# Kernel tuning notes

Measured on AMD Instinct MI355X. Metric: run time of the kernel, lower is better.

Reference implementation:

```python
import jax, jax.numpy as jnp
import numpy as np

KNOTS = 17  # integration points on [0, 3]


def _buffers():
    t = jnp.linspace(0.0, 3.0, KNOTS, dtype=jnp.float32)
    dt = 3.0 / (KNOTS - 1)
    w = jnp.full((KNOTS,), 2.0 * dt, dtype=jnp.float32)
    w = w.at[0].set(dt).at[-1].set(dt)          # trapezoid-style end weights
    phi = jnp.exp(-jnp.square(t) / 2.0)         # ideal Gaussian ECF
    return t, phi, w * phi


def setup_inputs() -> dict:
    key = jax.random.key(0)
    k1, k2 = jax.random.split(key)
    N, D, P = 8192, 512, 1024
    z = jax.random.normal(k1, (N, D), dtype=jnp.float32)
    A = jax.random.normal(k2, (D, P), dtype=jnp.float32)  # random projections (hoisted from forward)
    return {"z": z, "A": A}


def reference(z, A):
    t, phi, weights = _buffers()
    D = z.shape[-1]
    flat = z.reshape(-1, D).astype(jnp.float32)            # [N, D]
    An = A / jnp.clip(jnp.linalg.norm(A, axis=0, keepdims=True), 1e-8)
    proj = flat @ An                                       # [N, P]
    x_t = proj[:, :, None] * t                             # [N, P, K]
    cos_mean = jnp.mean(jnp.cos(x_t), axis=0)              # [P, K]
    sin_mean = jnp.mean(jnp.sin(x_t), axis=0)              # [P, K]
    err = jnp.square(cos_mean - phi) + jnp.square(sin_mean)
    statistic = (err @ weights) * flat.shape[0]            # [P]
    return jnp.mean(statistic)
```

## Files before the change

### kernel.cpp

```cpp
#include <hip/hip_runtime.h>
#include <stdint.h>

#define N_SAMP 8192
#define D_DIM  512
#define P_DIM  1024
#define DT     0.1875f

typedef float f32x4 __attribute__((ext_vector_type(4)));
typedef float f32x2 __attribute__((ext_vector_type(2)));
typedef short bf16x8 __attribute__((ext_vector_type(8)));
typedef unsigned short u16;

__device__ __forceinline__ u16 f2bf(float x){
    unsigned int u = __float_as_uint(x);
    return (u16)((u + 0x7FFFu + ((u >> 16) & 1u)) >> 16);
}

__device__ __forceinline__ void load_lds16(const void* g, void* l){
    __builtin_amdgcn_global_load_lds(
        (const __attribute__((address_space(1))) void*)(uintptr_t)g,
        (__attribute__((address_space(3))) void*)(uint32_t)(uintptr_t)l,
        16, 0, 0);
}

__global__ __launch_bounds__(256) void k_zconv(const float4* __restrict__ z4,
                                               u16* __restrict__ zb,
                                               float* __restrict__ out){
    int i = blockIdx.x * 256 + threadIdx.x;
    if (i == 0) out[0] = 0.f;
    float4 v = z4[i];
    ushort4 o;
    o.x = f2bf(v.x); o.y = f2bf(v.y); o.z = f2bf(v.z); o.w = f2bf(v.w);
    ((ushort4*)zb)[i] = o;
}

__global__ __launch_bounds__(256) void k_norm(const float* __restrict__ A,
                                              float* __restrict__ inv){
    const float4* A4 = (const float4*)A;
    const int tid = threadIdx.x;
    const int q = tid & 7;
    const int g = tid >> 3;
    const int c = (blockIdx.x << 3) + q;
    float sx = 0.f, sy = 0.f, sz = 0.f, sw = 0.f;
    #pragma unroll 4
    for (int dd = 0; dd < 16; ++dd){
        float4 v = A4[(size_t)(g * 16 + dd) * 256 + c];
        sx += v.x * v.x; sy += v.y * v.y; sz += v.z * v.z; sw += v.w * v.w;
    }
    __shared__ float red[8][32][4];
    red[q][g][0] = sx; red[q][g][1] = sy; red[q][g][2] = sz; red[q][g][3] = sw;
    __syncthreads();
    if (tid < 32){
        int qq = tid >> 2, comp = tid & 3;
        float s = 0.f;
        #pragma unroll
        for (int gg = 0; gg < 32; ++gg) s += red[qq][gg][comp];
        float nrm = fmaxf(sqrtf(s), 1e-8f);
        inv[(c - q + qq) * 4 + comp] = 1.0f / nrm;
    }
}

__global__ __launch_bounds__(256) void k_trans(const float* __restrict__ A,
                                               const float* __restrict__ inv,
                                               u16* __restrict__ AnT){
    __shared__ float tile[32][33];
    int p0 = (blockIdx.x & 31) * 32;
    int d0 = (blockIdx.x >> 5) * 32;
    int tx = threadIdx.x & 31, ty = threadIdx.x >> 5;
    #pragma unroll
    for (int j = 0; j < 4; ++j){
        int dd = ty + j * 8;
        tile[dd][tx] = A[(size_t)(d0 + dd) * P_DIM + p0 + tx];
    }
    __syncthreads();
    #pragma unroll
    for (int j = 0; j < 4; ++j){
        int pp = ty + j * 8;
        float s = inv[p0 + pp];
        AnT[(size_t)(p0 + pp) * D_DIM + d0 + tx] = f2bf(tile[tx][pp] * s);
    }
}

__global__ __launch_bounds__(256) void k_gemm_ecf(const u16* __restrict__ zb,
                                                  const u16* __restrict__ AnT,
                                                  float* __restrict__ partial){
    __shared__ uint4 smem4[4096];
    const int tid = threadIdx.x;
    const int bm = blockIdx.x >> 3, bn = blockIdx.x & 7;
    const int m0 = bm << 7, n0 = bn << 7;
    const int w = tid >> 6, lane = tid & 63;
    const int r = lane & 15, kg = lane >> 4;
    const int wm = (w >> 1) << 6, wn = (w & 1) << 6;

    const int srow = tid >> 3;
    const int gsw  = ((tid & 7) ^ (srow & 7)) << 3;
    const u16* gA = zb  + (size_t)(m0 + srow) * D_DIM + gsw;
    const u16* gB = AnT + (size_t)(n0 + srow) * D_DIM + gsw;
    char* lbase = (char*)smem4 + w * 1024;

    f32x4 acc[4][4] = {};

    #pragma unroll
    for (int i = 0; i < 4; ++i){
        load_lds16(gA + (size_t)i * 32 * D_DIM, lbase + i * 4096);
        load_lds16(gB + (size_t)i * 32 * D_DIM, lbase + 16384 + i * 4096);
    }

    for (int kt = 0; kt < 8; ++kt){
        const int cur = kt & 1;
        __syncthreads();
        if (kt < 7){
            char* la = lbase + ((kt + 1) & 1) * 32768;
            #pragma unroll
            for (int i = 0; i < 4; ++i){
                load_lds16(gA + (size_t)i * 32 * D_DIM + (kt + 1) * 64, la + i * 4096);
                load_lds16(gB + (size_t)i * 32 * D_DIM + (kt + 1) * 64, la + 16384 + i * 4096);
            }
        }
        const u16* Ab = (const u16*)smem4 + cur * 16384;
        const u16* Bb = Ab + 8192;
        #pragma unroll
        for (int ks = 0; ks < 2; ++ks){
            bf16x8 af[4], bfr[4];
            #pragma unroll
            for (int i = 0; i < 4; ++i)
                af[i] = *(const bf16x8*)&Ab[(wm + i * 16 + r) * 64 +
                                            (((ks * 4 + kg) ^ (r & 7)) << 3)];
            #pragma unroll
            for (int j = 0; j < 4; ++j)
                bfr[j] = *(const bf16x8*)&Bb[(wn + j * 16 + r) * 64 +
                                             (((ks * 4 + kg) ^ (r & 7)) << 3)];
            #pragma unroll
            for (int i = 0; i < 4; ++i)
                #pragma unroll
                for (int j = 0; j < 4; ++j)
                    acc[i][j] = __builtin_amdgcn_mfma_f32_16x16x32_bf16(
                        af[i], bfr[j], acc[i][j], 0, 0, 0);
        }
    }

    __syncthreads();
    float* epil = (float*)smem4;
    #pragma unroll
    for (int jn = 0; jn < 4; ++jn){
        f32x2 sum[16];
        #pragma unroll
        for (int k = 0; k < 16; ++k) sum[k] = (f32x2){0.f, 0.f};
        #pragma unroll
        for (int i = 0; i < 4; ++i){
            #pragma unroll
            for (int q = 0; q < 4; ++q){
                float x = acc[i][jn][q] * DT;
                float c1 = __cosf(x), s1 = __sinf(x);
                float tc = c1 + c1;
                f32x2 prev = {1.f, 0.f};
                f32x2 curv = {c1, s1};
                sum[0] += curv;
                #pragma unroll
                for (int k = 2; k <= 16; ++k){
                    f32x2 nxt = tc * curv - prev;
                    sum[k - 1] += nxt;
                    prev = curv; curv = nxt;
                }
            }
        }
        #pragma unroll
        for (int k = 0; k < 16; ++k){
            f32x2 o;
            o.x = __shfl_xor(sum[k].x, 16); o.y = __shfl_xor(sum[k].y, 16);
            sum[k] += o;
            o.x = __shfl_xor(sum[k].x, 32); o.y = __shfl_xor(sum[k].y, 32);
            sum[k] += o;
        }
        if (lane < 16){
            const int cl = jn * 16 + lane;
            #pragma unroll
            for (int k = 0; k < 16; ++k){
                epil[(w * 32 + k)      * 64 + cl] = sum[k].x;
                epil[(w * 32 + 16 + k) * 64 + cl] = sum[k].y;
            }
        }
    }
    __syncthreads();
    for (int f0 = 0; f0 < 4096; f0 += 256){
        int f = f0 + tid;
        int cl = f & 127, j = f >> 7;
        int whi = cl >> 6, cll = cl & 63;
        float v = epil[(whi * 32 + j) * 64 + cll] +
                  epil[((whi + 2) * 32 + j) * 64 + cll];
        partial[((size_t)bm * 32 + j) * 1024 + n0 + cl] = v;
    }
}

__global__ __launch_bounds__(256) void k_reduce(const float* __restrict__ partial,
                                                float* __restrict__ out){
    const int tid = threadIdx.x;
    const int idx = blockIdx.x * 256 + tid;
    const int p = idx & 1023, j = idx >> 10;
    float s = 0.f;
    #pragma unroll 4
    for (int slot = 0; slot < 64; ++slot)
        s += partial[((size_t)slot * 32 + j) * 1024 + p];
    const int k = (j & 15) + 1;
    float tk = (float)k * DT;
    float phik = expf(-0.5f * tk * tk);
    float wk = ((k == 16) ? DT : 2.f * DT) * phik;
    float mean = s * (1.f / (float)N_SAMP);
    float diff = (j < 16) ? (mean - phik) : mean;
    float term = diff * diff * wk;
    #pragma unroll
    for (int o = 32; o > 0; o >>= 1) term += __shfl_xor(term, o);
    __shared__ float red[4];
    if ((tid & 63) == 0) red[tid >> 6] = term;
    __syncthreads();
    if (tid == 0)
        atomicAdd(out, (red[0] + red[1] + red[2] + red[3]) *
                       ((float)N_SAMP / (float)P_DIM));
}

extern "C" void kernel_launch(void* const* d_in, const int* in_sizes, int n_in,
                              void* d_out, int out_size, void* d_ws, size_t ws_size,
                              hipStream_t stream){
    const float* z = (const float*)d_in[0];
    const float* A = (const float*)d_in[1];
    char* ws = (char*)d_ws;
    float* inv     = (float*)(ws);
    u16*   AnT     = (u16*)  (ws + 8192);
    u16*   zb      = (u16*)  (ws + 1056768);
    float* partial = (float*)(ws + 9445376);
    float* out     = (float*)d_out;

    hipLaunchKernelGGL(k_zconv,    dim3(4096), dim3(256), 0, stream,
                       (const float4*)z, zb, out);
    hipLaunchKernelGGL(k_norm,     dim3(32),   dim3(256), 0, stream, A, inv);
    hipLaunchKernelGGL(k_trans,    dim3(512),  dim3(256), 0, stream, A, inv, AnT);
    hipLaunchKernelGGL(k_gemm_ecf, dim3(512),  dim3(256), 0, stream, zb, AnT, partial);
    hipLaunchKernelGGL(k_reduce,   dim3(128),  dim3(256), 0, stream, partial, out);
}
```

Measured before the change: 49.76 us.

## Fuse prep kernels, load B fragments directly from global, split reduce across lanes

Merges the z conversion, column-norm and transpose kernels into one launch, with 32 extra blocks each computing norms for 32 columns and transposing them, which removes two kernel launches and the inv round trip. The GEMM now reads B fragments straight from global memory (L2-resident AnT) into registers instead of staging them through LDS, halving shared memory use to allow more resident blocks. The reduce kernel splits each 64-slot sum across 4 lanes with shuffles and 4x the blocks for more parallelism. The risks are that direct global B loads add latency inside the MFMA loop, and that the 32 norm+transpose blocks each loop over all of D and may become the tail of the prep kernel.

Result: slower. 60.71 us (+22.0%).

```diff
diff --git a/kernel.cpp b/kernel.cpp
--- a/kernel.cpp
+++ b/kernel.cpp
@@ -23,68 +23,61 @@
         16, 0, 0);
 }
 
-__global__ __launch_bounds__(256) void k_zconv(const float4* __restrict__ z4,
-                                               u16* __restrict__ zb,
-                                               float* __restrict__ out){
-    int i = blockIdx.x * 256 + threadIdx.x;
-    if (i == 0) out[0] = 0.f;
-    float4 v = z4[i];
-    ushort4 o;
-    o.x = f2bf(v.x); o.y = f2bf(v.y); o.z = f2bf(v.z); o.w = f2bf(v.w);
-    ((ushort4*)zb)[i] = o;
-}
-
-__global__ __launch_bounds__(256) void k_norm(const float* __restrict__ A,
-                                              float* __restrict__ inv){
-    const float4* A4 = (const float4*)A;
+__global__ __launch_bounds__(256) void k_prep(const float4* __restrict__ z4,
+                                              u16* __restrict__ zb,
+                                              const float* __restrict__ A,
+                                              u16* __restrict__ AnT,
+                                              float* __restrict__ out){
     const int tid = threadIdx.x;
-    const int q = tid & 7;
-    const int g = tid >> 3;
-    const int c = (blockIdx.x << 3) + q;
-    float sx = 0.f, sy = 0.f, sz = 0.f, sw = 0.f;
-    #pragma unroll 4
-    for (int dd = 0; dd < 16; ++dd){
-        float4 v = A4[(size_t)(g * 16 + dd) * 256 + c];
-        sx += v.x * v.x; sy += v.y * v.y; sz += v.z * v.z; sw += v.w * v.w;
-    }
-    __shared__ float red[8][32][4];
-    red[q][g][0] = sx; red[q][g][1] = sy; red[q][g][2] = sz; red[q][g][3] = sw;
+    if (blockIdx.x < 4096){
+        int i = blockIdx.x * 256 + tid;
+        if (i == 0) out[0] = 0.f;
+        float4 v = z4[i];
+        ushort4 o;
+        o.x = f2bf(v.x); o.y = f2bf(v.y); o.z = f2bf(v.z); o.w = f2bf(v.w);
+        ((ushort4*)zb)[i] = o;
+        return;
+    }
+    __shared__ float tile[32][33];
+    __shared__ float red[8][32];
+    __shared__ float inv_s[32];
+    const int p0 = (blockIdx.x - 4096) * 32;
+    const int pl = tid & 31, dg = tid >> 5;
+    float s = 0.f;
+    #pragma unroll 8
+    for (int i = 0; i < 64; ++i){
+        float v = A[(size_t)(dg + 8 * i) * P_DIM + p0 + pl];
+        s += v * v;
+    }
+    red[dg][pl] = s;
     __syncthreads();
     if (tid < 32){
-        int qq = tid >> 2, comp = tid & 3;
-        float s = 0.f;
-        #pragma unroll
-        for (int gg = 0; gg < 32; ++gg) s += red[qq][gg][comp];
-        float nrm = fmaxf(sqrtf(s), 1e-8f);
-        inv[(c - q + qq) * 4 + comp] = 1.0f / nrm;
-    }
-}
-
-__global__ __launch_bounds__(256) void k_trans(const float* __restrict__ A,
-                                               const float* __restrict__ inv,
-                                               u16* __restrict__ AnT){
-    __shared__ float tile[32][33];
-    int p0 = (blockIdx.x & 31) * 32;
-    int d0 = (blockIdx.x >> 5) * 32;
-    int tx = threadIdx.x & 31, ty = threadIdx.x >> 5;
-    #pragma unroll
-    for (int j = 0; j < 4; ++j){
-        int dd = ty + j * 8;
-        tile[dd][tx] = A[(size_t)(d0 + dd) * P_DIM + p0 + tx];
-    }
-    __syncthreads();
-    #pragma unroll
-    for (int j = 0; j < 4; ++j){
-        int pp = ty + j * 8;
-        float s = inv[p0 + pp];
-        AnT[(size_t)(p0 + pp) * D_DIM + d0 + tx] = f2bf(tile[tx][pp] * s);
+        float t = 0.f;
+        #pragma unroll
+        for (int g = 0; g < 8; ++g) t += red[g][tid];
+        inv_s[tid] = 1.0f / fmaxf(sqrtf(t), 1e-8f);
+    }
+    __syncthreads();
+    for (int dt = 0; dt < 16; ++dt){
+        #pragma unroll
+        for (int ii = 0; ii < 4; ++ii)
+            tile[dg + ii * 8][pl] =
+                A[(size_t)(dt * 32 + dg + ii * 8) * P_DIM + p0 + pl];
+        __syncthreads();
+        #pragma unroll
+        for (int ii = 0; ii < 4; ++ii){
+            int pr = dg + ii * 8;
+            AnT[(size_t)(p0 + pr) * D_DIM + dt * 32 + pl] =
+                f2bf(tile[pl][pr] * inv_s[pr]);
+        }
+        __syncthreads();
     }
 }
 
 __global__ __launch_bounds__(256) void k_gemm_ecf(const u16* __restrict__ zb,
                                                   const u16* __restrict__ AnT,
                                                   float* __restrict__ partial){
-    __shared__ uint4 smem4[4096];
+    __shared__ uint4 smem4[2048];
     const int tid = threadIdx.x;
     const int bm = blockIdx.x >> 3, bn = blockIdx.x & 7;
     const int m0 = bm << 7, n0 = bn << 7;
@@ -94,48 +87,48 @@
 
     const int srow = tid >> 3;
     const int gsw  = ((tid & 7) ^ (srow & 7)) << 3;
-    const u16* gA = zb  + (size_t)(m0 + srow) * D_DIM + gsw;
-    const u16* gB = AnT + (size_t)(n0 + srow) * D_DIM + gsw;
+    const u16* gA = zb + (size_t)(m0 + srow) * D_DIM + gsw;
     char* lbase = (char*)smem4 + w * 1024;
 
+    const u16* gB = AnT + (size_t)(n0 + wn + r) * D_DIM + kg * 8;
+
     f32x4 acc[4][4] = {};
 
     #pragma unroll
-    for (int i = 0; i < 4; ++i){
+    for (int i = 0; i < 4; ++i)
         load_lds16(gA + (size_t)i * 32 * D_DIM, lbase + i * 4096);
-        load_lds16(gB + (size_t)i * 32 * D_DIM, lbase + 16384 + i * 4096);
-    }
 
     for (int kt = 0; kt < 8; ++kt){
         const int cur = kt & 1;
         __syncthreads();
         if (kt < 7){
-            char* la = lbase + ((kt + 1) & 1) * 32768;
-            #pragma unroll
-            for (int i = 0; i < 4; ++i){
-                load_lds16(gA + (size_t)i * 32 * D_DIM + (kt + 1) * 64, la + i * 4096);
-                load_lds16(gB + (size_t)i * 32 * D_DIM + (kt + 1) * 64, la + 16384 + i * 4096);
-            }
-        }
-        const u16* Ab = (const u16*)smem4 + cur * 16384;
-        const u16* Bb = Ab + 8192;
+            char* la = lbase + ((kt + 1) & 1) * 16384;
+            #pragma unroll
+            for (int i = 0; i < 4; ++i)
+                load_lds16(gA + (size_t)i * 32 * D_DIM + (kt + 1) * 64,
+                           la + i * 4096);
+        }
+        bf16x8 bfr[2][4];
+        #pragma unroll
+        for (int ks = 0; ks < 2; ++ks)
+            #pragma unroll
+            for (int j = 0; j < 4; ++j)
+                bfr[ks][j] = *(const bf16x8*)&gB[(size_t)j * 16 * D_DIM +
+                                                 kt * 64 + ks * 32];
+        const u16* Ab = (const u16*)smem4 + cur * 8192;
         #pragma unroll
         for (int ks = 0; ks < 2; ++ks){
-            bf16x8 af[4], bfr[4];
+            bf16x8 af[4];
             #pragma unroll
             for (int i = 0; i < 4; ++i)
                 af[i] = *(const bf16x8*)&Ab[(wm + i * 16 + r) * 64 +
                                             (((ks * 4 + kg) ^ (r & 7)) << 3)];
-            #pragma unroll
-            for (int j = 0; j < 4; ++j)
-                bfr[j] = *(const bf16x8*)&Bb[(wn + j * 16 + r) * 64 +
-                                             (((ks * 4 + kg) ^ (r & 7)) << 3)];
             #pragma unroll
             for (int i = 0; i < 4; ++i)
                 #pragma unroll
                 for (int j = 0; j < 4; ++j)
                     acc[i][j] = __builtin_amdgcn_mfma_f32_16x16x32_bf16(
-                        af[i], bfr[j], acc[i][j], 0, 0, 0);
+                        af[i], bfr[ks][j], acc[i][j], 0, 0, 0);
         }
     }
 
@@ -195,12 +188,15 @@
 __global__ __launch_bounds__(256) void k_reduce(const float* __restrict__ partial,
                                                 float* __restrict__ out){
     const int tid = threadIdx.x;
-    const int idx = blockIdx.x * 256 + tid;
-    const int p = idx & 1023, j = idx >> 10;
+    const int gt = blockIdx.x * 256 + tid;
+    const int pair = gt >> 2, quarter = gt & 3;
+    const int p = pair & 1023, j = pair >> 10;
     float s = 0.f;
-    #pragma unroll 4
-    for (int slot = 0; slot < 64; ++slot)
-        s += partial[((size_t)slot * 32 + j) * 1024 + p];
+    #pragma unroll
+    for (int i = 0; i < 16; ++i)
+        s += partial[((size_t)(quarter * 16 + i) * 32 + j) * 1024 + p];
+    s += __shfl_xor(s, 1);
+    s += __shfl_xor(s, 2);
     const int k = (j & 15) + 1;
     float tk = (float)k * DT;
     float phik = expf(-0.5f * tk * tk);
@@ -214,7 +210,7 @@
     if ((tid & 63) == 0) red[tid >> 6] = term;
     __syncthreads();
     if (tid == 0)
-        atomicAdd(out, (red[0] + red[1] + red[2] + red[3]) *
+        atomicAdd(out, (red[0] + red[1] + red[2] + red[3]) * 0.25f *
                        ((float)N_SAMP / (float)P_DIM));
 }
 
@@ -224,16 +220,13 @@
     const float* z = (const float*)d_in[0];
     const float* A = (const float*)d_in[1];
     char* ws = (char*)d_ws;
-    float* inv     = (float*)(ws);
     u16*   AnT     = (u16*)  (ws + 8192);
     u16*   zb      = (u16*)  (ws + 1056768);
     float* partial = (float*)(ws + 9445376);
     float* out     = (float*)d_out;
 
-    hipLaunchKernelGGL(k_zconv,    dim3(4096), dim3(256), 0, stream,
-                       (const float4*)z, zb, out);
-    hipLaunchKernelGGL(k_norm,     dim3(32),   dim3(256), 0, stream, A, inv);
-    hipLaunchKernelGGL(k_trans,    dim3(512),  dim3(256), 0, stream, A, inv, AnT);
+    hipLaunchKernelGGL(k_prep,     dim3(4128), dim3(256), 0, stream,
+                       (const float4*)z, zb, A, AnT, out);
     hipLaunchKernelGGL(k_gemm_ecf, dim3(512),  dim3(256), 0, stream, zb, AnT, partial);
-    hipLaunchKernelGGL(k_reduce,   dim3(128),  dim3(256), 0, stream, partial, out);
-}
+    hipLaunchKernelGGL(k_reduce,   dim3(512),  dim3(256), 0, stream, partial, out);
+}
```

## Fuse z conversion with column-norm kernel, swizzle GEMM blocks, widen reduce

Applied to the files above, without the earlier changes.

Combines the z bf16 conversion and the column-norm computation into a single launch. Extra blocks in that launch handle 32 projection columns each, using scalar coalesced loads. The GEMM block index is remapped so that consecutive blocks share the same column tile (bn), which is meant to improve L2 reuse of AnT. The reduce kernel splits its 64-slot sum across 4 threads joined by shuffles and uses 4x more blocks, adding a 0.25 factor to undo the resulting replicated terms. The aim is to save one launch and raise parallelism, but the duplicated term accumulation changes rounding slightly.

Result: slower. 50.86 us (+2.2%).

```diff
diff --git a/kernel.cpp b/kernel.cpp
--- a/kernel.cpp
+++ b/kernel.cpp
@@ -23,40 +23,37 @@
         16, 0, 0);
 }
 
-__global__ __launch_bounds__(256) void k_zconv(const float4* __restrict__ z4,
+__global__ __launch_bounds__(256) void k_prep0(const float4* __restrict__ z4,
                                                u16* __restrict__ zb,
+                                               const float* __restrict__ A,
+                                               float* __restrict__ inv,
                                                float* __restrict__ out){
-    int i = blockIdx.x * 256 + threadIdx.x;
-    if (i == 0) out[0] = 0.f;
-    float4 v = z4[i];
-    ushort4 o;
-    o.x = f2bf(v.x); o.y = f2bf(v.y); o.z = f2bf(v.z); o.w = f2bf(v.w);
-    ((ushort4*)zb)[i] = o;
-}
-
-__global__ __launch_bounds__(256) void k_norm(const float* __restrict__ A,
-                                              float* __restrict__ inv){
-    const float4* A4 = (const float4*)A;
     const int tid = threadIdx.x;
-    const int q = tid & 7;
-    const int g = tid >> 3;
-    const int c = (blockIdx.x << 3) + q;
-    float sx = 0.f, sy = 0.f, sz = 0.f, sw = 0.f;
-    #pragma unroll 4
-    for (int dd = 0; dd < 16; ++dd){
-        float4 v = A4[(size_t)(g * 16 + dd) * 256 + c];
-        sx += v.x * v.x; sy += v.y * v.y; sz += v.z * v.z; sw += v.w * v.w;
-    }
-    __shared__ float red[8][32][4];
-    red[q][g][0] = sx; red[q][g][1] = sy; red[q][g][2] = sz; red[q][g][3] = sw;
+    if (blockIdx.x < 4096){
+        int i = blockIdx.x * 256 + tid;
+        if (i == 0) out[0] = 0.f;
+        float4 v = z4[i];
+        ushort4 o;
+        o.x = f2bf(v.x); o.y = f2bf(v.y); o.z = f2bf(v.z); o.w = f2bf(v.w);
+        ((ushort4*)zb)[i] = o;
+        return;
+    }
+    __shared__ float red[8][32];
+    const int p0 = (blockIdx.x - 4096) * 32;
+    const int pl = tid & 31, dg = tid >> 5;
+    float s = 0.f;
+    #pragma unroll 8
+    for (int i = 0; i < 64; ++i){
+        float v = A[(size_t)(dg + 8 * i) * P_DIM + p0 + pl];
+        s += v * v;
+    }
+    red[dg][pl] = s;
     __syncthreads();
     if (tid < 32){
-        int qq = tid >> 2, comp = tid & 3;
-        float s = 0.f;
-        #pragma unroll
-        for (int gg = 0; gg < 32; ++gg) s += red[qq][gg][comp];
-        float nrm = fmaxf(sqrtf(s), 1e-8f);
-        inv[(c - q + qq) * 4 + comp] = 1.0f / nrm;
+        float t = 0.f;
+        #pragma unroll
+        for (int g = 0; g < 8; ++g) t += red[g][tid];
+        inv[p0 + tid] = 1.0f / fmaxf(sqrtf(t), 1e-8f);
     }
 }
 
@@ -86,7 +83,8 @@
                                                   float* __restrict__ partial){
     __shared__ uint4 smem4[4096];
     const int tid = threadIdx.x;
-    const int bm = blockIdx.x >> 3, bn = blockIdx.x & 7;
+    const int swz = (blockIdx.x & 7) * 64 + (blockIdx.x >> 3);
+    const int bm = swz >> 3, bn = swz & 7;
     const int m0 = bm << 7, n0 = bn << 7;
     const int w = tid >> 6, lane = tid & 63;
     const int r = lane & 15, kg = lane >> 4;
@@ -195,12 +193,15 @@
 __global__ __launch_bounds__(256) void k_reduce(const float* __restrict__ partial,
                                                 float* __restrict__ out){
     const int tid = threadIdx.x;
-    const int idx = blockIdx.x * 256 + tid;
-    const int p = idx & 1023, j = idx >> 10;
+    const int gt = blockIdx.x * 256 + tid;
+    const int pair = gt >> 2, quarter = gt & 3;
+    const int p = pair & 1023, j = pair >> 10;
     float s = 0.f;
-    #pragma unroll 4
-    for (int slot = 0; slot < 64; ++slot)
-        s += partial[((size_t)slot * 32 + j) * 1024 + p];
+    #pragma unroll
+    for (int i = 0; i < 16; ++i)
+        s += partial[((size_t)(quarter * 16 + i) * 32 + j) * 1024 + p];
+    s += __shfl_xor(s, 1);
+    s += __shfl_xor(s, 2);
     const int k = (j & 15) + 1;
     float tk = (float)k * DT;
     float phik = expf(-0.5f * tk * tk);
@@ -214,7 +215,7 @@
     if ((tid & 63) == 0) red[tid >> 6] = term;
     __syncthreads();
     if (tid == 0)
-        atomicAdd(out, (red[0] + red[1] + red[2] + red[3]) *
+        atomicAdd(out, (red[0] + red[1] + red[2] + red[3]) * 0.25f *
                        ((float)N_SAMP / (float)P_DIM));
 }
 
@@ -230,10 +231,9 @@
     float* partial = (float*)(ws + 9445376);
     float* out     = (float*)d_out;
 
-    hipLaunchKernelGGL(k_zconv,    dim3(4096), dim3(256), 0, stream,
-                       (const float4*)z, zb, out);
-    hipLaunchKernelGGL(k_norm,     dim3(32),   dim3(256), 0, stream, A, inv);
+    hipLaunchKernelGGL(k_prep0,    dim3(4128), dim3(256), 0, stream,
+                       (const float4*)z, zb, A, inv, out);
     hipLaunchKernelGGL(k_trans,    dim3(512),  dim3(256), 0, stream, A, inv, AnT);
     hipLaunchKernelGGL(k_gemm_ecf, dim3(512),  dim3(256), 0, stream, zb, AnT, partial);
-    hipLaunchKernelGGL(k_reduce,   dim3(128),  dim3(256), 0, stream, partial, out);
-}
+    hipLaunchKernelGGL(k_reduce,   dim3(512),  dim3(256), 0, stream, partial, out);
+}
```
